# Performance work log

Measured on AMD Instinct MI355X. Metric: run time of the kernel, lower is better.

## Reference

```python
import jax, jax.numpy as jnp
import numpy as np

NUM_GROUPS = 32
EPS = 1e-6


def group_norm(x, scale, bias):
    # x: [B, C, H, W]
    B, C, H, W = x.shape
    g = x.reshape(B, NUM_GROUPS, C // NUM_GROUPS, H, W)
    mean = g.mean(axis=(2, 3, 4), keepdims=True)
    var = g.var(axis=(2, 3, 4), keepdims=True)
    g = (g - mean) * jax.lax.rsqrt(var + EPS)
    x = g.reshape(B, C, H, W)
    return x * scale[None, :, None, None] + bias[None, :, None, None]


def nin(x, W, b):
    # 1x1 projection over channel dim: x [B,C,H,W], W [C,D], b [D]
    return jnp.einsum('bchw,cd->bdhw', x, W) + b[None, :, None, None]


def setup_inputs() -> dict:
    key = jax.random.key(0)
    ks = jax.random.split(key, 8)
    B, C, H, W = 32, 512, 32, 32
    # xavier_uniform bound for [C, C]
    bound = float(np.sqrt(6.0 / (C + C)))

    def xavier(k):
        return jax.random.uniform(k, (C, C), jnp.float32, -bound, bound)

    return {
        'x': jax.random.normal(ks[0], (B, C, H, W), jnp.float32),
        'gn_scale': jnp.ones((C,), jnp.float32),
        'gn_bias': jnp.zeros((C,), jnp.float32),
        'Wq': xavier(ks[1]), 'bq': jnp.zeros((C,), jnp.float32),
        'Wk': xavier(ks[2]), 'bk': jnp.zeros((C,), jnp.float32),
        'Wv': xavier(ks[3]), 'bv': jnp.zeros((C,), jnp.float32),
        'Wt': xavier(ks[4]), 'bt': jnp.zeros((C,), jnp.float32),
    }


def reference(x, gn_scale, gn_bias, Wq, bq, Wk, bk, Wv, bv, Wt, bt):
    B, C, H, W = x.shape
    h = group_norm(x, gn_scale, gn_bias)
    q = nin(h, Wq, bq)
    k = nin(h, Wk, bk)
    v = nin(h, Wv, bv)
    # full attention over H*W tokens
    w = jnp.einsum('bchw,bcij->bhwij', q, k) * (C ** -0.5)
    w = jax.nn.softmax(w.reshape(B, H, W, H * W), axis=-1).reshape(B, H, W, H, W)
    h = jnp.einsum('bhwij,bcij->bchw', w, v)
    h = nin(h, Wt, bt)
    return h + x
```

## Files before the change

kernel.cpp:

```cpp
#include <hip/hip_runtime.h>
#include <stdint.h>

#define Bsz 32
#define Cch 512
#define Ssp 1024
#define Grp 32
#define CPG 16

typedef unsigned short u16;
typedef __attribute__((ext_vector_type(8))) short bf16x8;
typedef __attribute__((ext_vector_type(4))) float f32x4;

__device__ __forceinline__ float bf2f(u16 u) {
  union { float f; uint32_t i; } w; w.i = ((uint32_t)u) << 16; return w.f;
}
__device__ __forceinline__ u16 f2bf(float f) {
  union { float f; uint32_t i; } w; w.f = f;
  uint32_t r = w.i + 0x7fffu + ((w.i >> 16) & 1u);
  return (u16)(r >> 16);
}

__device__ __forceinline__ void gload_lds16(const u16* g, u16* l) {
  __builtin_amdgcn_global_load_lds(
      (const __attribute__((address_space(1))) uint32_t*)g,
      (__attribute__((address_space(3))) uint32_t*)l, 16, 0, 0);
}

__global__ __launch_bounds__(256) void gnstats_kernel(
    const float* __restrict__ x, const float* __restrict__ scale,
    const float* __restrict__ bias, float2* __restrict__ stats) {
  int b = blockIdx.x >> 5;
  int g = blockIdx.x & 31;
  size_t base = ((size_t)b * Cch + (size_t)g * CPG) * Ssp;
  const float4* xv = (const float4*)(x + base);

  float sum = 0.f, sumsq = 0.f;
#pragma unroll
  for (int it = 0; it < 16; ++it) {
    float4 v = xv[threadIdx.x + 256 * it];
    sum += (v.x + v.y) + (v.z + v.w);
    sumsq += (v.x * v.x + v.y * v.y) + (v.z * v.z + v.w * v.w);
  }
#pragma unroll
  for (int off = 32; off > 0; off >>= 1) {
    sum += __shfl_xor(sum, off);
    sumsq += __shfl_xor(sumsq, off);
  }
  __shared__ float sm[8];
  int wid = threadIdx.x >> 6;
  if ((threadIdx.x & 63) == 0) { sm[wid] = sum; sm[4 + wid] = sumsq; }
  __syncthreads();
  sum = sm[0] + sm[1] + sm[2] + sm[3];
  sumsq = sm[4] + sm[5] + sm[6] + sm[7];
  float mean = sum * (1.f / 16384.f);
  float var = sumsq * (1.f / 16384.f) - mean * mean;
  float rstd = rsqrtf(var + 1e-6f);
  if (threadIdx.x < CPG) {
    int c = g * CPG + threadIdx.x;
    float sc = scale[c] * rstd;
    stats[(size_t)b * Cch + c] = make_float2(sc, bias[c] - mean * sc);
  }
}

__global__ __launch_bounds__(256) void xpose_gn(
    const float* __restrict__ x, const float2* __restrict__ stats,
    u16* __restrict__ xt) {
  __shared__ float T[64][65];
  int b = blockIdx.z;
  int s0 = blockIdx.x * 64, c0 = blockIdx.y * 64;
  int t = threadIdx.x;
  {
    int tx = t & 15, ty = t >> 4;
    const float* xb = x + ((size_t)b * Cch + c0) * Ssp + s0;
#pragma unroll
    for (int i = 0; i < 4; ++i) {
      int c = ty + 16 * i;
      float2 af = stats[(size_t)b * Cch + c0 + c];
      float4 v = *(const float4*)&xb[(size_t)c * Ssp + tx * 4];
      T[c][tx * 4 + 0] = v.x * af.x + af.y;
      T[c][tx * 4 + 1] = v.y * af.x + af.y;
      T[c][tx * 4 + 2] = v.z * af.x + af.y;
      T[c][tx * 4 + 3] = v.w * af.x + af.y;
    }
  }
  __syncthreads();
  {
    int cx = t & 7, sy = t >> 3;
    u16* ob = xt + ((size_t)b * Ssp + s0) * Cch + c0;
#pragma unroll
    for (int i = 0; i < 2; ++i) {
      int s = sy + 32 * i;
      union { u16 h[8]; uint4 v4; } pk;
#pragma unroll
      for (int j = 0; j < 8; ++j) pk.h[j] = f2bf(T[cx * 8 + j][s]);
      *(uint4*)&ob[(size_t)s * Cch + cx * 8] = pk.v4;
    }
  }
}

__global__ __launch_bounds__(256) void wxpose(
    const float* __restrict__ w0, const float* __restrict__ w1,
    const float* __restrict__ w2, const float* __restrict__ w3,
    u16* __restrict__ dst) {
  const float* W = blockIdx.z == 0 ? w0 : blockIdx.z == 1 ? w1
                   : blockIdx.z == 2 ? w2 : w3;
  u16* D = dst + (size_t)blockIdx.z * Cch * Cch;
  __shared__ float T[64][65];
  int d0 = blockIdx.x * 64, c0 = blockIdx.y * 64;
  int t = threadIdx.x;
  {
    int tx = t & 15, ty = t >> 4;
#pragma unroll
    for (int i = 0; i < 4; ++i) {
      int c = ty + 16 * i;
      float4 v = *(const float4*)&W[(size_t)(c0 + c) * Cch + d0 + tx * 4];
      T[c][tx * 4 + 0] = v.x; T[c][tx * 4 + 1] = v.y;
      T[c][tx * 4 + 2] = v.z; T[c][tx * 4 + 3] = v.w;
    }
  }
  __syncthreads();
  {
    int cx = t & 7, dy = t >> 3;
#pragma unroll
    for (int i = 0; i < 2; ++i) {
      int d = dy + 32 * i;
      union { u16 h[8]; uint4 v4; } pk;
#pragma unroll
      for (int j = 0; j < 8; ++j) pk.h[j] = f2bf(T[cx * 8 + j][d]);
      *(uint4*)&D[(size_t)(d0 + d) * Cch + c0 + cx * 8] = pk.v4;
    }
  }
}

template <int EPI>
__global__ __launch_bounds__(256) void mfma_nt(
    const u16* __restrict__ A, size_t sAb, int lda,
    const u16* __restrict__ B, size_t sBb, int ldb,
    void* __restrict__ Out, size_t sOb, int ldo,
    const float* __restrict__ bias,
    const float* __restrict__ bias2_or_resid, size_t sRb, int K) {
  __shared__ u16 As[2 * 4096];
  __shared__ u16 Bs[2 * 4096];

  const int nx = gridDim.x, ny = gridDim.y;
  const int pb = nx * ny;
  const int nwg = pb * gridDim.z;
  const int flat = (blockIdx.z * ny + blockIdx.y) * nx + blockIdx.x;
  const int qq = nwg >> 3, rr = nwg & 7;
  const int xcd = flat & 7, lid = flat >> 3;
  const int nf = (xcd < rr ? xcd * (qq + 1) : rr * (qq + 1) + (xcd - rr) * qq) + lid;
  const int b = nf / pb;
  const int rem = nf - b * pb;
  const int m0 = (rem / nx) * 128, n0 = (rem % nx) * 128;

  const int tid = threadIdx.x;
  const int lane = tid & 63, wave = tid >> 6;
  const int wm = wave >> 1, wn = wave & 1;
  const int quad = lane >> 4, l16 = lane & 15;

  const int sp = lane & 7, sq = lane >> 3;
  const int scl = sp ^ sq;
  const int srow = 2 * sq + (scl >> 2);
  const int scol = (scl & 3) * 8;

  const u16* Ab = A + (size_t)b * sAb + (size_t)m0 * lda;
  const u16* Bb = B + (size_t)b * sBb + (size_t)n0 * ldb;

  f32x4 acc[4][4] = {};

#define STAGE(bufidx, kk)                                                      \
  {                                                                            \
    _Pragma("unroll") for (int i = 0; i < 2; ++i) {                            \
      int seg = 2 * wave + i;                                                  \
      gload_lds16(Ab + (size_t)(16 * seg + srow) * lda + (kk) + scol,          \
                  As + (bufidx) * 4096 + seg * 512);                           \
      gload_lds16(Bb + (size_t)(16 * seg + srow) * ldb + (kk) + scol,          \
                  Bs + (bufidx) * 4096 + seg * 512);                           \
    }                                                                          \
  }

  STAGE(0, 0)
  __syncthreads();
  int cur = 0;
  for (int k0 = 0; k0 < K; k0 += 32) {
    if (k0 + 32 < K) STAGE(cur ^ 1, k0 + 32)
    bf16x8 af[4], bfr[4];
#pragma unroll
    for (int i = 0; i < 4; ++i) {
      int ra = wm * 64 + i * 16 + l16;
      int qa = ra >> 1, ca = ((ra & 1) << 2) + quad;
      af[i] = *(const bf16x8*)&As[cur * 4096 + qa * 64 + (ca ^ (qa & 7)) * 8];
      int rb = wn * 64 + i * 16 + l16;
      int qb = rb >> 1, cb = ((rb & 1) << 2) + quad;
      bfr[i] = *(const bf16x8*)&Bs[cur * 4096 + qb * 64 + (cb ^ (qb & 7)) * 8];
    }
#pragma unroll
    for (int mt = 0; mt < 4; ++mt)
#pragma unroll
      for (int nt = 0; nt < 4; ++nt)
        acc[mt][nt] = __builtin_amdgcn_mfma_f32_16x16x32_bf16(
            af[mt], bfr[nt], acc[mt][nt], 0, 0, 0);
    __syncthreads();
    cur ^= 1;
  }
#undef STAGE

  const float SCALE = 0.044194173824159216f;
#pragma unroll
  for (int mt = 0; mt < 4; ++mt) {
#pragma unroll
    for (int nt = 0; nt < 4; ++nt) {
      int n = n0 + wn * 64 + nt * 16 + l16;
      float bn = 0.f;
      if constexpr (EPI == 0)
        bn = (n < 512) ? bias[n] : bias2_or_resid[n - 512];
#pragma unroll
      for (int reg = 0; reg < 4; ++reg) {
        int m = m0 + wm * 64 + mt * 16 + quad * 4 + reg;
        float v = acc[mt][nt][reg];
        size_t idx = (size_t)b * sOb + (size_t)m * ldo + n;
        if constexpr (EPI == 0) {
          ((u16*)Out)[idx] = f2bf(v + bn);
        } else if constexpr (EPI == 1) {
          ((u16*)Out)[idx] = f2bf(v + bias[m]);
        } else if constexpr (EPI == 2) {
          ((u16*)Out)[idx] = f2bf(v * SCALE);
        } else if constexpr (EPI == 3) {
          ((u16*)Out)[idx] = f2bf(v);
        } else {
          ((float*)Out)[idx] =
              v + bias[m] + bias2_or_resid[(size_t)b * sRb + (size_t)m * ldo + n];
        }
      }
    }
  }
}

__global__ __launch_bounds__(256) void softmax_kernel(u16* __restrict__ Sc) {
  size_t row = blockIdx.x;
  u16* rp = Sc + row * (size_t)Ssp;
  uint2 u = ((const uint2*)rp)[threadIdx.x];
  const u16* ph = (const u16*)&u;
  float v0 = bf2f(ph[0]), v1 = bf2f(ph[1]), v2 = bf2f(ph[2]), v3 = bf2f(ph[3]);
  float mx = fmaxf(fmaxf(v0, v1), fmaxf(v2, v3));
#pragma unroll
  for (int off = 32; off > 0; off >>= 1) mx = fmaxf(mx, __shfl_xor(mx, off));
  __shared__ float sm[4];
  __shared__ float sd[4];
  int wid = threadIdx.x >> 6;
  if ((threadIdx.x & 63) == 0) sm[wid] = mx;
  __syncthreads();
  mx = fmaxf(fmaxf(sm[0], sm[1]), fmaxf(sm[2], sm[3]));
  float e0 = __expf(v0 - mx), e1 = __expf(v1 - mx);
  float e2 = __expf(v2 - mx), e3 = __expf(v3 - mx);
  float s = e0 + e1 + e2 + e3;
#pragma unroll
  for (int off = 32; off > 0; off >>= 1) s += __shfl_xor(s, off);
  if ((threadIdx.x & 63) == 0) sd[wid] = s;
  __syncthreads();
  s = sd[0] + sd[1] + sd[2] + sd[3];
  float inv = 1.f / s;
  union { u16 s4[4]; uint2 v2; } pk;
  pk.s4[0] = f2bf(e0 * inv); pk.s4[1] = f2bf(e1 * inv);
  pk.s4[2] = f2bf(e2 * inv); pk.s4[3] = f2bf(e3 * inv);
  ((uint2*)rp)[threadIdx.x] = pk.v2;
}

extern "C" void kernel_launch(void* const* d_in, const int* in_sizes, int n_in,
                              void* d_out, int out_size, void* d_ws, size_t ws_size,
                              hipStream_t stream) {
  (void)in_sizes; (void)n_in; (void)out_size;
  const float* x   = (const float*)d_in[0];
  const float* gns = (const float*)d_in[1];
  const float* gnb = (const float*)d_in[2];
  const float* Wq  = (const float*)d_in[3];
  const float* bq  = (const float*)d_in[4];
  const float* Wk  = (const float*)d_in[5];
  const float* bk  = (const float*)d_in[6];
  const float* Wv  = (const float*)d_in[7];
  const float* bv  = (const float*)d_in[8];
  const float* Wt  = (const float*)d_in[9];
  const float* bt  = (const float*)d_in[10];
  float* out = (float*)d_out;
  char* ws = (char*)d_ws;

  const size_t QKSZ = (size_t)Bsz * Ssp * 1024 * 2;
  u16* qkt = (u16*)ws;
  u16* vv  = (u16*)(ws + QKSZ);
  u16* Wts = (u16*)(ws + (96ull << 20));
  float2* stats = (float2*)(ws + (98ull << 20));
  u16* xt  = (u16*)(ws + (99ull << 20));
  u16* Sc  = xt;
  u16* ot  = qkt;

  int NB;
  if (ws_size >= (163ull << 20)) NB = 32;
  else if (ws_size >= (131ull << 20)) NB = 16;
  else NB = 8;

  const size_t WSZ = (size_t)Cch * Cch;
  u16* Wvt = Wts + 2 * WSZ;
  u16* Wtt = Wts + 3 * WSZ;

  const size_t sSC  = (size_t)Ssp * Cch;
  const size_t sQK  = (size_t)Ssp * 1024;
  const size_t sCS  = (size_t)Cch * Ssp;
  const size_t sScB = (size_t)Ssp * Ssp;
  dim3 blk(256);

  gnstats_kernel<<<dim3(Bsz * Grp), blk, 0, stream>>>(x, gns, gnb, stats);
  xpose_gn<<<dim3(Ssp / 64, Cch / 64, Bsz), blk, 0, stream>>>(x, stats, xt);
  wxpose<<<dim3(8, 8, 4), blk, 0, stream>>>(Wq, Wk, Wv, Wt, Wts);

  mfma_nt<0><<<dim3(8, 8, Bsz), blk, 0, stream>>>(
      xt, sSC, Cch, Wts, 0, Cch, qkt, sQK, 1024, bq, bk, 0, Cch);
  mfma_nt<1><<<dim3(8, 4, Bsz), blk, 0, stream>>>(
      Wvt, 0, Cch, xt, sSC, Cch, vv, sCS, Ssp, bv, nullptr, 0, Cch);

  for (int b0 = 0; b0 < Bsz; b0 += NB) {
    int nb = (b0 + NB <= Bsz) ? NB : (Bsz - b0);
    mfma_nt<2><<<dim3(8, 8, nb), blk, 0, stream>>>(
        qkt + b0 * sQK, sQK, 1024, qkt + b0 * sQK + 512, sQK, 1024,
        Sc, sScB, Ssp, nullptr, nullptr, 0, Cch);
    softmax_kernel<<<dim3(nb * Ssp), blk, 0, stream>>>(Sc);
    mfma_nt<3><<<dim3(4, 8, nb), blk, 0, stream>>>(
        Sc, sScB, Ssp, vv + b0 * sCS, sCS, Ssp,
        ot + b0 * sSC, sSC, Cch, nullptr, nullptr, 0, Ssp);
  }

  mfma_nt<4><<<dim3(8, 4, Bsz), blk, 0, stream>>>(
      Wtt, 0, Cch, ot, sSC, Cch, out, sCS, Ssp, bt, x, sCS, Cch);
}
```

Baseline: 373.2 us.

## Add 256x256-tile 8-wave MFMA GEMM for QK projection and score GEMMs

Adds a new GEMM kernel using 512 threads (8 waves) and 256x256 output tiles, double-buffered LDS staging through global_load_lds, swizzled LDS reads, XCD-aware block remapping, and s_setprio around MFMA bursts. It replaces the 128-tile kernel for the Q/K projection and the QK^T score GEMM. The larger tiles raise arithmetic intensity and cut global traffic per FLOP, at the cost of 128KB of LDS per block, heavy register use that limits occupancy, and fewer blocks, which can hurt wave balance.

```diff
diff --git a/kernel.cpp b/kernel.cpp
--- a/kernel.cpp
+++ b/kernel.cpp
@@ -236,6 +236,141 @@
   }
 }
 
+template <int EPI>
+__global__ __launch_bounds__(512, 2) void mfma_nt8(
+    const u16* __restrict__ A, size_t sAb, int lda,
+    const u16* __restrict__ B, size_t sBb, int ldb,
+    void* __restrict__ Out, size_t sOb, int ldo,
+    const float* __restrict__ bias,
+    const float* __restrict__ bias2, int K) {
+  __shared__ u16 As[2 * 16384];
+  __shared__ u16 Bs[2 * 16384];
+
+  const int nx = gridDim.x, ny = gridDim.y;
+  const int pb = nx * ny;
+  const int nwg = pb * gridDim.z;
+  const int flat = (blockIdx.z * ny + blockIdx.y) * nx + blockIdx.x;
+  const int qq = nwg >> 3, rr = nwg & 7;
+  const int xcd = flat & 7, lid = flat >> 3;
+  const int nf = (xcd < rr ? xcd * (qq + 1) : rr * (qq + 1) + (xcd - rr) * qq) + lid;
+  const int b = nf / pb;
+  const int rem = nf - b * pb;
+  const int m0 = (rem / nx) * 256, n0 = (rem % nx) * 256;
+
+  const int tid = threadIdx.x;
+  const int lane = tid & 63, wave = tid >> 6;
+  const int wm = wave >> 2, wn = wave & 3;
+  const int quad = lane >> 4, l16 = lane & 15;
+
+  const int sp = lane & 7, sq = lane >> 3;
+  const int scl = sp ^ sq;
+  const int srow = 2 * sq + (scl >> 2);
+  const int scol = (scl & 3) * 8;
+
+  const int vbase = ((l16 >> 1) << 6) + ((((l16 & 1) << 2) | quad) ^ (l16 >> 1)) * 8;
+  const int aw = wm * 8192;
+  const int bw = (wn >> 1) * 8192 + (wn & 1) * 2048;
+
+  const u16* Ab = A + (size_t)b * sAb + (size_t)m0 * lda;
+  const u16* Bb = B + (size_t)b * sBb + (size_t)n0 * ldb;
+
+  f32x4 acc[8][4] = {};
+
+#define STAGE8(bufidx, kt)                                                     \
+  {                                                                            \
+    _Pragma("unroll") for (int i = 0; i < 4; ++i) {                            \
+      int gs = wave * 4 + i;                                                   \
+      int row = ((gs >> 4) << 7) + ((gs & 7) << 4) + srow;                     \
+      int kof = (kt) * 64 + (((gs >> 3) & 1) << 5) + scol;                     \
+      gload_lds16(Ab + (size_t)row * lda + kof,                                \
+                  As + (bufidx) * 16384 + gs * 512);                           \
+      gload_lds16(Bb + (size_t)row * ldb + kof,                                \
+                  Bs + (bufidx) * 16384 + gs * 512);                           \
+    }                                                                          \
+  }
+
+  STAGE8(0, 0)
+  asm volatile("s_waitcnt vmcnt(0)" ::: "memory");
+  asm volatile("s_barrier" ::: "memory");
+
+  const int nk = K >> 6;
+  for (int kt = 0; kt < nk; ++kt) {
+    const int cur = kt & 1;
+    if (kt + 1 < nk) {
+      STAGE8(cur ^ 1, kt + 1)
+      asm volatile("s_waitcnt vmcnt(8)" ::: "memory");
+    } else {
+      asm volatile("s_waitcnt vmcnt(0)" ::: "memory");
+    }
+    asm volatile("s_barrier" ::: "memory");
+
+    bf16x8 bfv[4][2], af[4][2];
+#pragma unroll
+    for (int nfr = 0; nfr < 4; ++nfr)
+#pragma unroll
+      for (int kr = 0; kr < 2; ++kr)
+        bfv[nfr][kr] = *(const bf16x8*)&Bs[cur * 16384 + bw + kr * 4096 +
+                                           nfr * 512 + vbase];
+#pragma unroll
+    for (int mf = 0; mf < 4; ++mf)
+#pragma unroll
+      for (int kr = 0; kr < 2; ++kr)
+        af[mf][kr] = *(const bf16x8*)&As[cur * 16384 + aw + kr * 4096 +
+                                         mf * 512 + vbase];
+    __builtin_amdgcn_s_setprio(1);
+#pragma unroll
+    for (int mf = 0; mf < 4; ++mf)
+#pragma unroll
+      for (int nfr = 0; nfr < 4; ++nfr)
+#pragma unroll
+        for (int kr = 0; kr < 2; ++kr)
+          acc[mf][nfr] = __builtin_amdgcn_mfma_f32_16x16x32_bf16(
+              af[mf][kr], bfv[nfr][kr], acc[mf][nfr], 0, 0, 0);
+    __builtin_amdgcn_s_setprio(0);
+    asm volatile("s_barrier" ::: "memory");
+#pragma unroll
+    for (int mf = 0; mf < 4; ++mf)
+#pragma unroll
+      for (int kr = 0; kr < 2; ++kr)
+        af[mf][kr] = *(const bf16x8*)&As[cur * 16384 + aw + kr * 4096 +
+                                         (4 + mf) * 512 + vbase];
+    __builtin_amdgcn_s_setprio(1);
+#pragma unroll
+    for (int mf = 0; mf < 4; ++mf)
+#pragma unroll
+      for (int nfr = 0; nfr < 4; ++nfr)
+#pragma unroll
+        for (int kr = 0; kr < 2; ++kr)
+          acc[4 + mf][nfr] = __builtin_amdgcn_mfma_f32_16x16x32_bf16(
+              af[mf][kr], bfv[nfr][kr], acc[4 + mf][nfr], 0, 0, 0);
+    __builtin_amdgcn_s_setprio(0);
+    asm volatile("s_barrier" ::: "memory");
+  }
+#undef STAGE8
+
+  const float SCALE = 0.044194173824159216f;
+#pragma unroll
+  for (int mf = 0; mf < 8; ++mf) {
+#pragma unroll
+    for (int nfr = 0; nfr < 4; ++nfr) {
+      int n = n0 + wn * 64 + nfr * 16 + l16;
+      float bn = 0.f;
+      if constexpr (EPI == 0) bn = (n < 512) ? bias[n] : bias2[n - 512];
+#pragma unroll
+      for (int reg = 0; reg < 4; ++reg) {
+        int m = m0 + wm * 128 + mf * 16 + quad * 4 + reg;
+        float v = acc[mf][nfr][reg];
+        size_t idx = (size_t)b * sOb + (size_t)m * ldo + n;
+        if constexpr (EPI == 0) {
+          ((u16*)Out)[idx] = f2bf(v + bn);
+        } else {
+          ((u16*)Out)[idx] = f2bf(v * SCALE);
+        }
+      }
+    }
+  }
+}
+
 __global__ __launch_bounds__(256) void softmax_kernel(u16* __restrict__ Sc) {
   size_t row = blockIdx.x;
   u16* rp = Sc + row * (size_t)Ssp;
@@ -307,21 +442,22 @@
   const size_t sCS  = (size_t)Cch * Ssp;
   const size_t sScB = (size_t)Ssp * Ssp;
   dim3 blk(256);
+  dim3 blk8(512);
 
   gnstats_kernel<<<dim3(Bsz * Grp), blk, 0, stream>>>(x, gns, gnb, stats);
   xpose_gn<<<dim3(Ssp / 64, Cch / 64, Bsz), blk, 0, stream>>>(x, stats, xt);
   wxpose<<<dim3(8, 8, 4), blk, 0, stream>>>(Wq, Wk, Wv, Wt, Wts);
 
-  mfma_nt<0><<<dim3(8, 8, Bsz), blk, 0, stream>>>(
-      xt, sSC, Cch, Wts, 0, Cch, qkt, sQK, 1024, bq, bk, 0, Cch);
+  mfma_nt8<0><<<dim3(4, 4, Bsz), blk8, 0, stream>>>(
+      xt, sSC, Cch, Wts, 0, Cch, qkt, sQK, 1024, bq, bk, Cch);
   mfma_nt<1><<<dim3(8, 4, Bsz), blk, 0, stream>>>(
       Wvt, 0, Cch, xt, sSC, Cch, vv, sCS, Ssp, bv, nullptr, 0, Cch);
 
   for (int b0 = 0; b0 < Bsz; b0 += NB) {
     int nb = (b0 + NB <= Bsz) ? NB : (Bsz - b0);
-    mfma_nt<2><<<dim3(8, 8, nb), blk, 0, stream>>>(
+    mfma_nt8<2><<<dim3(4, 4, nb), blk8, 0, stream>>>(
         qkt + b0 * sQK, sQK, 1024, qkt + b0 * sQK + 512, sQK, 1024,
-        Sc, sScB, Ssp, nullptr, nullptr, 0, Cch);
+        Sc, sScB, Ssp, nullptr, nullptr, Cch);
     softmax_kernel<<<dim3(nb * Ssp), blk, 0, stream>>>(Sc);
     mfma_nt<3><<<dim3(4, 8, nb), blk, 0, stream>>>(
         Sc, sScB, Ssp, vv + b0 * sCS, sCS, Ssp,
```

Result: slower. 382.1 us (+2.4%).

## Switch GEMMs to 256x128 tiles, 512 threads, triple-buffered LDS pipeline

Applied to the files above, without the earlier changes.

Replaces the 128x128, 256-thread double-buffered GEMM with a 256x128-tile, 8-wave kernel that keeps three LDS stages in flight. It uses explicit vmcnt waits and raw barriers instead of __syncthreads, and raises wave priority around the MFMA block. The goal is to hide global-to-LDS latency better and to reuse each B tile across more rows, cutting loads per FLOP. The cost is more LDS per block (72 KB) and half as many workgroups, which may lower occupancy and tail balance on small grids.

```diff
diff --git a/kernel.cpp b/kernel.cpp
--- a/kernel.cpp
+++ b/kernel.cpp
@@ -133,14 +133,14 @@
 }
 
 template <int EPI>
-__global__ __launch_bounds__(256) void mfma_nt(
+__global__ __launch_bounds__(512, 4) void mfma_nt3(
     const u16* __restrict__ A, size_t sAb, int lda,
     const u16* __restrict__ B, size_t sBb, int ldb,
     void* __restrict__ Out, size_t sOb, int ldo,
     const float* __restrict__ bias,
     const float* __restrict__ bias2_or_resid, size_t sRb, int K) {
-  __shared__ u16 As[2 * 4096];
-  __shared__ u16 Bs[2 * 4096];
+  __shared__ u16 As[3 * 8192];
+  __shared__ u16 Bs[3 * 4096];
 
   const int nx = gridDim.x, ny = gridDim.y;
   const int pb = nx * ny;
@@ -151,7 +151,7 @@
   const int nf = (xcd < rr ? xcd * (qq + 1) : rr * (qq + 1) + (xcd - rr) * qq) + lid;
   const int b = nf / pb;
   const int rem = nf - b * pb;
-  const int m0 = (rem / nx) * 128, n0 = (rem % nx) * 128;
+  const int m0 = (rem / nx) * 256, n0 = (rem % nx) * 128;
 
   const int tid = threadIdx.x;
   const int lane = tid & 63, wave = tid >> 6;
@@ -163,61 +163,85 @@
   const int srow = 2 * sq + (scl >> 2);
   const int scol = (scl & 3) * 8;
 
+  const int vbase =
+      ((l16 >> 1) << 6) + ((((l16 & 1) << 2) | quad) ^ (l16 >> 1)) * 8;
+
   const u16* Ab = A + (size_t)b * sAb + (size_t)m0 * lda;
   const u16* Bb = B + (size_t)b * sBb + (size_t)n0 * ldb;
 
+  const int gsa0 = 2 * wave, gsa1 = 2 * wave + 1;
+  const u16* pA0 =
+      Ab + (size_t)(((gsa0 >> 3) << 7) + ((gsa0 & 7) << 4) + srow) * lda + scol;
+  const u16* pA1 =
+      Ab + (size_t)(((gsa1 >> 3) << 7) + ((gsa1 & 7) << 4) + srow) * lda + scol;
+  const u16* pB = Bb + (size_t)((wave << 4) + srow) * ldb + scol;
+  u16* lA0 = As + gsa0 * 512;
+  u16* lA1 = As + gsa1 * 512;
+  u16* lB = Bs + wave * 512;
+
+  const int aoff = (wm >> 1) * 4096 + (wm & 1) * 2048 + vbase;
+  const int boff = wn * 2048 + vbase;
+
   f32x4 acc[4][4] = {};
 
-#define STAGE(bufidx, kk)                                                      \
-  {                                                                            \
-    _Pragma("unroll") for (int i = 0; i < 2; ++i) {                            \
-      int seg = 2 * wave + i;                                                  \
-      gload_lds16(Ab + (size_t)(16 * seg + srow) * lda + (kk) + scol,          \
-                  As + (bufidx) * 4096 + seg * 512);                           \
-      gload_lds16(Bb + (size_t)(16 * seg + srow) * ldb + (kk) + scol,          \
-                  Bs + (bufidx) * 4096 + seg * 512);                           \
-    }                                                                          \
-  }
-
-  STAGE(0, 0)
-  __syncthreads();
+#define STAGE3(bufidx, kk)                             \
+  {                                                    \
+    gload_lds16(pA0 + (kk) * 32, lA0 + (bufidx) * 8192); \
+    gload_lds16(pA1 + (kk) * 32, lA1 + (bufidx) * 8192); \
+    gload_lds16(pB + (kk) * 32, lB + (bufidx) * 4096);   \
+  }
+
+  const int nk = K >> 5;
+  STAGE3(0, 0)
+  STAGE3(1, 1)
   int cur = 0;
-  for (int k0 = 0; k0 < K; k0 += 32) {
-    if (k0 + 32 < K) STAGE(cur ^ 1, k0 + 32)
-    bf16x8 af[4], bfr[4];
-#pragma unroll
-    for (int i = 0; i < 4; ++i) {
-      int ra = wm * 64 + i * 16 + l16;
-      int qa = ra >> 1, ca = ((ra & 1) << 2) + quad;
-      af[i] = *(const bf16x8*)&As[cur * 4096 + qa * 64 + (ca ^ (qa & 7)) * 8];
-      int rb = wn * 64 + i * 16 + l16;
-      int qb = rb >> 1, cb = ((rb & 1) << 2) + quad;
-      bfr[i] = *(const bf16x8*)&Bs[cur * 4096 + qb * 64 + (cb ^ (qb & 7)) * 8];
-    }
-#pragma unroll
-    for (int mt = 0; mt < 4; ++mt)
-#pragma unroll
-      for (int nt = 0; nt < 4; ++nt)
-        acc[mt][nt] = __builtin_amdgcn_mfma_f32_16x16x32_bf16(
-            af[mt], bfr[nt], acc[mt][nt], 0, 0, 0);
-    __syncthreads();
-    cur ^= 1;
-  }
-#undef STAGE
+  for (int kt = 0; kt < nk; ++kt) {
+    if (kt + 2 < nk) {
+      int stb = cur + 2;
+      if (stb >= 3) stb -= 3;
+      STAGE3(stb, kt + 2)
+      asm volatile("s_waitcnt vmcnt(6)" ::: "memory");
+    } else if (kt + 1 < nk) {
+      asm volatile("s_waitcnt vmcnt(3)" ::: "memory");
+    } else {
+      asm volatile("s_waitcnt vmcnt(0)" ::: "memory");
+    }
+    asm volatile("s_barrier" ::: "memory");
+
+    const u16* Asc = As + cur * 8192;
+    const u16* Bsc = Bs + cur * 4096;
+    bf16x8 bf[4];
+#pragma unroll
+    for (int nfr = 0; nfr < 4; ++nfr)
+      bf[nfr] = *(const bf16x8*)&Bsc[boff + nfr * 512];
+    __builtin_amdgcn_s_setprio(1);
+#pragma unroll
+    for (int mf = 0; mf < 4; ++mf) {
+      bf16x8 af = *(const bf16x8*)&Asc[aoff + mf * 512];
+#pragma unroll
+      for (int nfr = 0; nfr < 4; ++nfr)
+        acc[mf][nfr] = __builtin_amdgcn_mfma_f32_16x16x32_bf16(
+            af, bf[nfr], acc[mf][nfr], 0, 0, 0);
+    }
+    __builtin_amdgcn_s_setprio(0);
+    asm volatile("s_barrier" ::: "memory");
+    if (++cur == 3) cur = 0;
+  }
+#undef STAGE3
 
   const float SCALE = 0.044194173824159216f;
 #pragma unroll
-  for (int mt = 0; mt < 4; ++mt) {
-#pragma unroll
-    for (int nt = 0; nt < 4; ++nt) {
-      int n = n0 + wn * 64 + nt * 16 + l16;
+  for (int mf = 0; mf < 4; ++mf) {
+#pragma unroll
+    for (int nfr = 0; nfr < 4; ++nfr) {
+      int n = n0 + wn * 64 + nfr * 16 + l16;
       float bn = 0.f;
       if constexpr (EPI == 0)
         bn = (n < 512) ? bias[n] : bias2_or_resid[n - 512];
 #pragma unroll
       for (int reg = 0; reg < 4; ++reg) {
-        int m = m0 + wm * 64 + mt * 16 + quad * 4 + reg;
-        float v = acc[mt][nt][reg];
+        int m = m0 + wm * 64 + mf * 16 + quad * 4 + reg;
+        float v = acc[mf][nfr][reg];
         size_t idx = (size_t)b * sOb + (size_t)m * ldo + n;
         if constexpr (EPI == 0) {
           ((u16*)Out)[idx] = f2bf(v + bn);
@@ -307,27 +331,28 @@
   const size_t sCS  = (size_t)Cch * Ssp;
   const size_t sScB = (size_t)Ssp * Ssp;
   dim3 blk(256);
+  dim3 blk8(512);
 
   gnstats_kernel<<<dim3(Bsz * Grp), blk, 0, stream>>>(x, gns, gnb, stats);
   xpose_gn<<<dim3(Ssp / 64, Cch / 64, Bsz), blk, 0, stream>>>(x, stats, xt);
   wxpose<<<dim3(8, 8, 4), blk, 0, stream>>>(Wq, Wk, Wv, Wt, Wts);
 
-  mfma_nt<0><<<dim3(8, 8, Bsz), blk, 0, stream>>>(
+  mfma_nt3<0><<<dim3(8, 4, Bsz), blk8, 0, stream>>>(
       xt, sSC, Cch, Wts, 0, Cch, qkt, sQK, 1024, bq, bk, 0, Cch);
-  mfma_nt<1><<<dim3(8, 4, Bsz), blk, 0, stream>>>(
+  mfma_nt3<1><<<dim3(8, 2, Bsz), blk8, 0, stream>>>(
       Wvt, 0, Cch, xt, sSC, Cch, vv, sCS, Ssp, bv, nullptr, 0, Cch);
 
   for (int b0 = 0; b0 < Bsz; b0 += NB) {
     int nb = (b0 + NB <= Bsz) ? NB : (Bsz - b0);
-    mfma_nt<2><<<dim3(8, 8, nb), blk, 0, stream>>>(
+    mfma_nt3<2><<<dim3(8, 4, nb), blk8, 0, stream>>>(
         qkt + b0 * sQK, sQK, 1024, qkt + b0 * sQK + 512, sQK, 1024,
         Sc, sScB, Ssp, nullptr, nullptr, 0, Cch);
     softmax_kernel<<<dim3(nb * Ssp), blk, 0, stream>>>(Sc);
-    mfma_nt<3><<<dim3(4, 8, nb), blk, 0, stream>>>(
+    mfma_nt3<3><<<dim3(4, 4, nb), blk8, 0, stream>>>(
         Sc, sScB, Ssp, vv + b0 * sCS, sCS, Ssp,
         ot + b0 * sSC, sSC, Cch, nullptr, nullptr, 0, Ssp);
   }
 
-  mfma_nt<4><<<dim3(8, 4, Bsz), blk, 0, stream>>>(
+  mfma_nt3<4><<<dim3(8, 2, Bsz), blk8, 0, stream>>>(
       Wtt, 0, Cch, ot, sSC, Cch, out, sCS, Ssp, bt, x, sCS, Cch);
 }
```

New measurement: 358.7 us. -3.9%, faster.

## Switch GEMMs to 256x256 tiles with 8 waves and interleaved load/MFMA schedule

Applied to the files above, without the earlier changes.

Replaces the 128x128, 4-wave bf16 MFMA GEMM with a 256x256, 8-wave kernel that uses a K-step of 64. Global-to-LDS loads are split into four phases interleaved with MFMA blocks, using explicit barriers, waitcnt and setprio. The larger tile is meant to raise data reuse per LDS byte and overlap memory traffic with compute. In exchange it uses much more LDS (128KB) and more registers per block, and it gives smaller grids with fewer workgroups per batch.

```diff
diff --git a/kernel.cpp b/kernel.cpp
--- a/kernel.cpp
+++ b/kernel.cpp
@@ -133,14 +133,14 @@
 }
 
 template <int EPI>
-__global__ __launch_bounds__(256) void mfma_nt(
+__global__ __launch_bounds__(512, 2) void mfma_ntf(
     const u16* __restrict__ A, size_t sAb, int lda,
     const u16* __restrict__ B, size_t sBb, int ldb,
     void* __restrict__ Out, size_t sOb, int ldo,
     const float* __restrict__ bias,
     const float* __restrict__ bias2_or_resid, size_t sRb, int K) {
-  __shared__ u16 As[2 * 4096];
-  __shared__ u16 Bs[2 * 4096];
+  __shared__ u16 As[2 * 16384];
+  __shared__ u16 Bs[2 * 16384];
 
   const int nx = gridDim.x, ny = gridDim.y;
   const int pb = nx * ny;
@@ -148,14 +148,14 @@
   const int flat = (blockIdx.z * ny + blockIdx.y) * nx + blockIdx.x;
   const int qq = nwg >> 3, rr = nwg & 7;
   const int xcd = flat & 7, lid = flat >> 3;
-  const int nf = (xcd < rr ? xcd * (qq + 1) : rr * (qq + 1) + (xcd - rr) * qq) + lid;
-  const int b = nf / pb;
-  const int rem = nf - b * pb;
-  const int m0 = (rem / nx) * 128, n0 = (rem % nx) * 128;
+  const int nf2 = (xcd < rr ? xcd * (qq + 1) : rr * (qq + 1) + (xcd - rr) * qq) + lid;
+  const int b = nf2 / pb;
+  const int rem = nf2 - b * pb;
+  const int m0 = (rem / nx) * 256, n0 = (rem % nx) * 256;
 
   const int tid = threadIdx.x;
   const int lane = tid & 63, wave = tid >> 6;
-  const int wm = wave >> 1, wn = wave & 1;
+  const int wm = wave >> 2, wn = wave & 3;
   const int quad = lane >> 4, l16 = lane & 15;
 
   const int sp = lane & 7, sq = lane >> 3;
@@ -163,61 +163,122 @@
   const int srow = 2 * sq + (scl >> 2);
   const int scol = (scl & 3) * 8;
 
+  const int vbase =
+      ((l16 >> 1) << 6) + ((((l16 & 1) << 2) | quad) ^ (l16 >> 1)) * 8;
+
   const u16* Ab = A + (size_t)b * sAb + (size_t)m0 * lda;
   const u16* Bb = B + (size_t)b * sBb + (size_t)n0 * ldb;
 
-  f32x4 acc[4][4] = {};
-
-#define STAGE(bufidx, kk)                                                      \
+  f32x4 acc[8][4] = {};
+
+#define STG(p, kt1, nbuf)                                                      \
   {                                                                            \
-    _Pragma("unroll") for (int i = 0; i < 2; ++i) {                            \
-      int seg = 2 * wave + i;                                                  \
-      gload_lds16(Ab + (size_t)(16 * seg + srow) * lda + (kk) + scol,          \
-                  As + (bufidx) * 4096 + seg * 512);                           \
-      gload_lds16(Bb + (size_t)(16 * seg + srow) * ldb + (kk) + scol,          \
-                  Bs + (bufidx) * 4096 + seg * 512);                           \
-    }                                                                          \
-  }
-
-  STAGE(0, 0)
-  __syncthreads();
-  int cur = 0;
-  for (int k0 = 0; k0 < K; k0 += 32) {
-    if (k0 + 32 < K) STAGE(cur ^ 1, k0 + 32)
-    bf16x8 af[4], bfr[4];
-#pragma unroll
-    for (int i = 0; i < 4; ++i) {
-      int ra = wm * 64 + i * 16 + l16;
-      int qa = ra >> 1, ca = ((ra & 1) << 2) + quad;
-      af[i] = *(const bf16x8*)&As[cur * 4096 + qa * 64 + (ca ^ (qa & 7)) * 8];
-      int rb = wn * 64 + i * 16 + l16;
-      int qb = rb >> 1, cb = ((rb & 1) << 2) + quad;
-      bfr[i] = *(const bf16x8*)&Bs[cur * 4096 + qb * 64 + (cb ^ (qb & 7)) * 8];
-    }
-#pragma unroll
-    for (int mt = 0; mt < 4; ++mt)
-#pragma unroll
-      for (int nt = 0; nt < 4; ++nt)
-        acc[mt][nt] = __builtin_amdgcn_mfma_f32_16x16x32_bf16(
-            af[mt], bfr[nt], acc[mt][nt], 0, 0, 0);
-    __syncthreads();
-    cur ^= 1;
-  }
-#undef STAGE
+    const int u_ = wave * 4 + (p);                                             \
+    const int su_ = u_ & 15, kh_ = u_ >> 4;                                    \
+    gload_lds16(Ab + (size_t)(su_ * 16 + srow) * lda + (kt1) * 64 + kh_ * 32 + \
+                    scol,                                                      \
+                As + (nbuf) * 16384 + kh_ * 8192 + su_ * 512);                 \
+    gload_lds16(Bb + (size_t)(su_ * 16 + srow) * ldb + (kt1) * 64 + kh_ * 32 + \
+                    scol,                                                      \
+                Bs + (nbuf) * 16384 + kh_ * 8192 + su_ * 512);                 \
+  }
+
+#define LDA(mf, kk) \
+  (*(const bf16x8*)&As[cur * 16384 + (kk) * 8192 + (wm * 8 + (mf)) * 512 + vbase])
+#define LDB(nf, kk) \
+  (*(const bf16x8*)&Bs[cur * 16384 + (kk) * 8192 + (wn * 4 + (nf)) * 512 + vbase])
+
+#define BAR asm volatile("s_barrier" ::: "memory")
+#define WAIT_VM0 asm volatile("s_waitcnt vmcnt(0)" ::: "memory")
+#define WAIT_LGKM0                                    \
+  asm volatile("s_waitcnt lgkmcnt(0)" ::: "memory");  \
+  __builtin_amdgcn_sched_barrier(0)
+
+#pragma unroll
+  for (int p = 0; p < 4; ++p) STG(p, 0, 0)
+
+  const int nk = K >> 6;
+  bf16x8 b0[4], b1[4], a[4];
+  for (int kt = 0; kt < nk; ++kt) {
+    const int cur = kt & 1;
+    const int nbuf = cur ^ 1;
+    const bool nxt = (kt + 1 < nk);
+    WAIT_VM0;
+    BAR;
+#pragma unroll
+    for (int i = 0; i < 4; ++i) b0[i] = LDB(i, 0);
+#pragma unroll
+    for (int i = 0; i < 4; ++i) a[i] = LDA(i, 0);
+    if (nxt) STG(0, kt + 1, nbuf)
+    BAR;
+    WAIT_LGKM0;
+    __builtin_amdgcn_s_setprio(1);
+#pragma unroll
+    for (int mf = 0; mf < 4; ++mf)
+#pragma unroll
+      for (int nf = 0; nf < 4; ++nf)
+        acc[mf][nf] = __builtin_amdgcn_mfma_f32_16x16x32_bf16(
+            a[mf], b0[nf], acc[mf][nf], 0, 0, 0);
+    __builtin_amdgcn_s_setprio(0);
+#pragma unroll
+    for (int i = 0; i < 4; ++i) b1[i] = LDB(i, 1);
+#pragma unroll
+    for (int i = 0; i < 4; ++i) a[i] = LDA(i, 1);
+    if (nxt) STG(1, kt + 1, nbuf)
+    BAR;
+    WAIT_LGKM0;
+    __builtin_amdgcn_s_setprio(1);
+#pragma unroll
+    for (int mf = 0; mf < 4; ++mf)
+#pragma unroll
+      for (int nf = 0; nf < 4; ++nf)
+        acc[mf][nf] = __builtin_amdgcn_mfma_f32_16x16x32_bf16(
+            a[mf], b1[nf], acc[mf][nf], 0, 0, 0);
+    __builtin_amdgcn_s_setprio(0);
+#pragma unroll
+    for (int i = 0; i < 4; ++i) a[i] = LDA(4 + i, 0);
+    if (nxt) STG(2, kt + 1, nbuf)
+    BAR;
+    WAIT_LGKM0;
+    __builtin_amdgcn_s_setprio(1);
+#pragma unroll
+    for (int mf = 0; mf < 4; ++mf)
+#pragma unroll
+      for (int nf = 0; nf < 4; ++nf)
+        acc[4 + mf][nf] = __builtin_amdgcn_mfma_f32_16x16x32_bf16(
+            a[mf], b0[nf], acc[4 + mf][nf], 0, 0, 0);
+    __builtin_amdgcn_s_setprio(0);
+#pragma unroll
+    for (int i = 0; i < 4; ++i) a[i] = LDA(4 + i, 1);
+    if (nxt) STG(3, kt + 1, nbuf)
+    BAR;
+    WAIT_LGKM0;
+    __builtin_amdgcn_s_setprio(1);
+#pragma unroll
+    for (int mf = 0; mf < 4; ++mf)
+#pragma unroll
+      for (int nf = 0; nf < 4; ++nf)
+        acc[4 + mf][nf] = __builtin_amdgcn_mfma_f32_16x16x32_bf16(
+            a[mf], b1[nf], acc[4 + mf][nf], 0, 0, 0);
+    __builtin_amdgcn_s_setprio(0);
+  }
+#undef STG
+#undef LDA
+#undef LDB
 
   const float SCALE = 0.044194173824159216f;
 #pragma unroll
-  for (int mt = 0; mt < 4; ++mt) {
-#pragma unroll
-    for (int nt = 0; nt < 4; ++nt) {
-      int n = n0 + wn * 64 + nt * 16 + l16;
+  for (int mf = 0; mf < 8; ++mf) {
+#pragma unroll
+    for (int nf = 0; nf < 4; ++nf) {
+      int n = n0 + wn * 64 + nf * 16 + l16;
       float bn = 0.f;
       if constexpr (EPI == 0)
         bn = (n < 512) ? bias[n] : bias2_or_resid[n - 512];
 #pragma unroll
       for (int reg = 0; reg < 4; ++reg) {
-        int m = m0 + wm * 64 + mt * 16 + quad * 4 + reg;
-        float v = acc[mt][nt][reg];
+        int m = m0 + wm * 128 + mf * 16 + quad * 4 + reg;
+        float v = acc[mf][nf][reg];
         size_t idx = (size_t)b * sOb + (size_t)m * ldo + n;
         if constexpr (EPI == 0) {
           ((u16*)Out)[idx] = f2bf(v + bn);
@@ -307,27 +368,28 @@
   const size_t sCS  = (size_t)Cch * Ssp;
   const size_t sScB = (size_t)Ssp * Ssp;
   dim3 blk(256);
+  dim3 blk8(512);
 
   gnstats_kernel<<<dim3(Bsz * Grp), blk, 0, stream>>>(x, gns, gnb, stats);
   xpose_gn<<<dim3(Ssp / 64, Cch / 64, Bsz), blk, 0, stream>>>(x, stats, xt);
   wxpose<<<dim3(8, 8, 4), blk, 0, stream>>>(Wq, Wk, Wv, Wt, Wts);
 
-  mfma_nt<0><<<dim3(8, 8, Bsz), blk, 0, stream>>>(
+  mfma_ntf<0><<<dim3(4, 4, Bsz), blk8, 0, stream>>>(
       xt, sSC, Cch, Wts, 0, Cch, qkt, sQK, 1024, bq, bk, 0, Cch);
-  mfma_nt<1><<<dim3(8, 4, Bsz), blk, 0, stream>>>(
+  mfma_ntf<1><<<dim3(4, 2, Bsz), blk8, 0, stream>>>(
       Wvt, 0, Cch, xt, sSC, Cch, vv, sCS, Ssp, bv, nullptr, 0, Cch);
 
   for (int b0 = 0; b0 < Bsz; b0 += NB) {
     int nb = (b0 + NB <= Bsz) ? NB : (Bsz - b0);
-    mfma_nt<2><<<dim3(8, 8, nb), blk, 0, stream>>>(
+    mfma_ntf<2><<<dim3(4, 4, nb), blk8, 0, stream>>>(
         qkt + b0 * sQK, sQK, 1024, qkt + b0 * sQK + 512, sQK, 1024,
         Sc, sScB, Ssp, nullptr, nullptr, 0, Cch);
     softmax_kernel<<<dim3(nb * Ssp), blk, 0, stream>>>(Sc);
-    mfma_nt<3><<<dim3(4, 8, nb), blk, 0, stream>>>(
+    mfma_ntf<3><<<dim3(2, 4, nb), blk8, 0, stream>>>(
         Sc, sScB, Ssp, vv + b0 * sCS, sCS, Ssp,
         ot + b0 * sSC, sSC, Cch, nullptr, nullptr, 0, Ssp);
   }
 
-  mfma_nt<4><<<dim3(8, 4, Bsz), blk, 0, stream>>>(
+  mfma_ntf<4><<<dim3(4, 2, Bsz), blk8, 0, stream>>>(
       Wtt, 0, Cch, ot, sSC, Cch, out, sCS, Ssp, bt, x, sCS, Cch);
 }
```

Measured after the change: 355.4 us. 4.8% less time.
